# Kernel optimization log

Measured on AMD Instinct MI355X. Metric: run time of the kernel, lower is better.

The kernel has to match this reference:

```python
import jax, jax.numpy as jnp
import numpy as np

N_QUBITS = 6
N_LAYERS = 3
FEATURE_DIM = 512
ENC_HIDDEN = max(32, N_QUBITS * 4)  # 32
HEAD_HIDDEN = 128
G, T = 54, 24
DIM = 2 ** N_QUBITS  # 64


def _ry_batched(angles):
    # angles: [B] -> batched RY matrices [B, 2, 2] (complex64)
    c = jnp.cos(angles * 0.5)
    s = jnp.sin(angles * 0.5)
    U = jnp.stack([jnp.stack([c, -s], -1), jnp.stack([s, c], -1)], -2)
    return U.astype(jnp.complex64)


def _rot(phi, theta, omega):
    # PennyLane Rot = RZ(omega) RY(theta) RZ(phi); returns [2, 2] complex64
    c = jnp.cos(theta * 0.5).astype(jnp.complex64)
    s = jnp.sin(theta * 0.5).astype(jnp.complex64)
    ep = jnp.exp(-0.5j * (phi + omega).astype(jnp.complex64))  # e^{-i(phi+omega)/2}
    em = jnp.exp(-0.5j * (phi - omega).astype(jnp.complex64))  # e^{-i(phi-omega)/2}
    u00 = ep * c
    u01 = -jnp.conj(em) * s
    u10 = em * s
    u11 = jnp.conj(ep) * c
    return jnp.stack([jnp.stack([u00, u01]), jnp.stack([u10, u11])])


def _apply_1q_batched(state, U, q):
    # state: [B, 2^n]; U: [B, 2, 2] (per-sample gate, e.g. data-encoding RY)
    B = state.shape[0]
    st = state.reshape(B, 2 ** q, 2, -1)
    st = jnp.einsum('bij,bljr->blir', U, st)
    return st.reshape(B, -1)


def _apply_1q(state, U, q):
    # state: [B, 2^n]; U: [2, 2] shared across batch (trainable Rot)
    B = state.shape[0]
    st = state.reshape(B, 2 ** q, 2, -1)
    st = jnp.einsum('ij,bljr->blir', U, st)
    return st.reshape(B, -1)


def _apply_cnot(state, c, t):
    # state: [B, 2^n]; flip target axis where control bit == 1
    B = state.shape[0]
    st = state.reshape((B,) + (2,) * N_QUBITS)
    ax_c, ax_t = 1 + c, 1 + t
    s0 = jnp.take(st, 0, axis=ax_c)
    s1 = jnp.take(st, 1, axis=ax_c)
    s1 = jnp.flip(s1, axis=ax_t if ax_t < ax_c else ax_t - 1)
    st = jnp.stack([s0, s1], axis=ax_c)
    return st.reshape(B, -1)


def _expvals_z(state):
    # <Z_q> for every qubit: [B, n]
    B = state.shape[0]
    probs = (state.real ** 2 + state.imag ** 2).reshape((B,) + (2,) * N_QUBITS)
    outs = []
    for q in range(N_QUBITS):
        axes = tuple(i for i in range(1, N_QUBITS + 1) if i != q + 1)
        p = probs.sum(axes)  # [B, 2]
        outs.append(p[:, 0] - p[:, 1])
    return jnp.stack(outs, -1)


def _circuit(angles, q_weights):
    # angles: [B, n_qubits] float32; q_weights: [L, n, 3]
    B = angles.shape[0]
    state = jnp.zeros((B, DIM), jnp.complex64).at[:, 0].set(1.0)
    for layer in range(N_LAYERS):
        # data_reuploading=True -> re-encode every layer
        for q in range(N_QUBITS):
            state = _apply_1q_batched(state, _ry_batched(angles[:, q]), q)
        for q in range(N_QUBITS):
            w = q_weights[layer, q]
            state = _apply_1q(state, _rot(w[0], w[1], w[2]), q)
        for q in range(0, N_QUBITS - 1, 2):
            state = _apply_cnot(state, q, q + 1)
        for q in range(1, N_QUBITS - 1, 2):
            state = _apply_cnot(state, q, q + 1)
        state = _apply_cnot(state, N_QUBITS - 1, 0)  # n_qubits > 2
    return _expvals_z(state)


def setup_inputs() -> dict:
    key = jax.random.key(0)
    ks = jax.random.split(key, 10)
    B = 32768
    return {
        'x': jax.random.normal(ks[0], (B, FEATURE_DIM), jnp.float32),
        'enc_w1': 0.05 * jax.random.normal(ks[1], (FEATURE_DIM, ENC_HIDDEN), jnp.float32),
        'enc_b1': jnp.zeros((ENC_HIDDEN,), jnp.float32),
        'enc_w2': 0.05 * jax.random.normal(ks[2], (ENC_HIDDEN, N_QUBITS), jnp.float32),
        'enc_b2': jnp.zeros((N_QUBITS,), jnp.float32),
        'q_weights': 0.01 * jax.random.normal(ks[3], (N_LAYERS, N_QUBITS, 3), jnp.float32),
        'head_w1': 0.1 * jax.random.normal(ks[4], (N_QUBITS, HEAD_HIDDEN), jnp.float32),
        'head_b1': jnp.zeros((HEAD_HIDDEN,), jnp.float32),
        'head_w2': 0.05 * jax.random.normal(ks[5], (HEAD_HIDDEN, G * T), jnp.float32),
        'head_b2': jnp.zeros((G * T,), jnp.float32),
    }


def reference(x, enc_w1, enc_b1, enc_w2, enc_b2, q_weights,
              head_w1, head_b1, head_w2, head_b2):
    # classical encoder -> angles [B, n_qubits]
    h = jnp.tanh(x @ enc_w1 + enc_b1)
    angles = h @ enc_w2 + enc_b2
    # batched state-vector PQC simulation
    z = _circuit(angles, q_weights).astype(jnp.float32)  # [B, n_qubits]
    # classical head (dropout is identity in eval)
    g = jax.nn.relu(z @ head_w1 + head_b1)
    logits = g @ head_w2 + head_b2
    return logits.reshape(-1, G, T)
```

## Files before the change

kernel.cpp:

```cpp
#include <hip/hip_runtime.h>

typedef __bf16 bf16x8 __attribute__((ext_vector_type(8)));
typedef float floatx4 __attribute__((ext_vector_type(4)));
typedef unsigned short ushort8 __attribute__((ext_vector_type(8)));

__device__ __forceinline__ unsigned short f2bf(float f) {
    unsigned u = __float_as_uint(f);
    u += 0x7fffu + ((u >> 16) & 1u);
    return (unsigned short)(u >> 16);
}

template <int ST>
__device__ __forceinline__ void apply_local(float* fr, float* fi,
    float m00r, float m00i, float m01r, float m01i,
    float m10r, float m10i, float m11r, float m11i) {
#pragma unroll
    for (int i = 0; i < 16; ++i) {
        if ((i & ST) == 0) {
            int i1 = i + ST;
            float r0 = fr[i], u0 = fi[i], r1 = fr[i1], u1 = fi[i1];
            fr[i]  = m00r * r0 - m00i * u0 + m01r * r1 - m01i * u1;
            fi[i]  = m00r * u0 + m00i * r0 + m01r * u1 + m01i * r1;
            fr[i1] = m10r * r0 - m10i * u0 + m11r * r1 - m11i * u1;
            fi[i1] = m10r * u0 + m10i * r0 + m11r * u1 + m11i * r1;
        }
    }
}

template <int XM>
__device__ __forceinline__ void apply_cross(float* fr, float* fi, bool hi,
    float m00r, float m00i, float m01r, float m01i,
    float m10r, float m10i, float m11r, float m11i) {
    float car = hi ? m10r : m00r, cai = hi ? m10i : m00i;
    float cbr = hi ? m11r : m01r, cbi = hi ? m11i : m01i;
#pragma unroll
    for (int j = 0; j < 16; ++j) {
        float mr = fr[j], mi = fi[j];
        float pr = __shfl_xor(mr, XM);
        float pi = __shfl_xor(mi, XM);
        float a0r = hi ? pr : mr, a0i = hi ? pi : mi;
        float a1r = hi ? mr : pr, a1i = hi ? mi : pi;
        fr[j] = car * a0r - cai * a0i + cbr * a1r - cbi * a1i;
        fi[j] = car * a0i + cai * a0r + cbr * a1i + cbi * a1r;
    }
}

#define SWAP2(a, b) { float _t = fr[a]; fr[a] = fr[b]; fr[b] = _t; \
                      _t = fi[a]; fi[a] = fi[b]; fi[b] = _t; }

__global__ __launch_bounds__(256) void fused_front(
    const float* __restrict__ x, const float* __restrict__ w1,
    const float* __restrict__ b1, const float* __restrict__ w2,
    const float* __restrict__ b2, const float* __restrict__ qw,
    const float* __restrict__ hw1, const float* __restrict__ hb1,
    const float* __restrict__ hw2,
    unsigned short* __restrict__ w2t, unsigned short* __restrict__ g) {

    if (blockIdx.x >= 512) {
        int t = (blockIdx.x - 512) * 256 + threadIdx.x;
        int nn = t >> 4;
        int kc = (t & 15) * 8;
        if (nn < 1296) {
            ushort8 pk;
#pragma unroll
            for (int j = 0; j < 8; ++j) pk[j] = f2bf(hw2[(size_t)(kc + j) * 1296 + nn]);
            *(ushort8*)(w2t + (size_t)nn * 128 + kc) = pk;
        }
        return;
    }

    __shared__ float part[4][64][33];
    __shared__ float hsh[64][33];
    __shared__ float umat_s[144];
    __shared__ float casa[64][12];

    if (threadIdx.x < 18) {
        int t = threadIdx.x;
        float phi = qw[t * 3], theta = qw[t * 3 + 1], omega = qw[t * 3 + 2];
        float c = cosf(0.5f * theta), s = sinf(0.5f * theta);
        float po = 0.5f * (phi + omega), pm = 0.5f * (phi - omega);
        float epr = cosf(po), epi = -sinf(po);
        float emr = cosf(pm), emi = -sinf(pm);
        float* u = umat_s + t * 8;
        u[0] = epr * c;  u[1] = epi * c;
        u[2] = -emr * s; u[3] = emi * s;
        u[4] = emr * s;  u[5] = emi * s;
        u[6] = epr * c;  u[7] = -epi * c;
    }

    int lane = threadIdx.x & 63;
    int wave = threadIdx.x >> 6;
    int swave = __builtin_amdgcn_readfirstlane(wave);
    size_t row = (size_t)blockIdx.x * 64 + lane;
    const float2* x2 = (const float2*)(x + row * 512 + swave * 128);
    const float* wseg = w1 + swave * 128 * 32;

    float acc[32];
#pragma unroll
    for (int j = 0; j < 32; ++j) acc[j] = 0.f;

#pragma clang loop unroll(disable)
    for (int k2 = 0; k2 < 64; ++k2) {
        float2 xv = x2[k2];
        const float* wr = wseg + k2 * 64;
#pragma unroll
        for (int j = 0; j < 32; ++j) acc[j] = fmaf(wr[j], xv.x, acc[j]);
#pragma unroll
        for (int j = 0; j < 32; ++j) acc[j] = fmaf(wr[32 + j], xv.y, acc[j]);
    }
#pragma unroll
    for (int j = 0; j < 32; ++j) part[wave][lane][j] = acc[j];
    __syncthreads();

    {
        int rl = threadIdx.x & 63;
        int jg = (threadIdx.x >> 6) * 8;
#pragma unroll
        for (int jj = 0; jj < 8; ++jj) {
            int j = jg + jj;
            float v = part[0][rl][j] + part[1][rl][j] + part[2][rl][j] + part[3][rl][j] + b1[j];
            hsh[rl][j] = tanhf(v);
        }
    }
    __syncthreads();

    {
        int row_a = threadIdx.x & 63;
        for (int qq = threadIdx.x >> 6; qq < 6; qq += 4) {
            float a = b2[qq];
#pragma unroll
            for (int j = 0; j < 32; ++j) a = fmaf(hsh[row_a][j], w2[j * 6 + qq], a);
            a *= 0.5f;
            casa[row_a][qq]     = cosf(a);
            casa[row_a][qq + 6] = sinf(a);
        }
    }
    __syncthreads();

    int samp = wave * 16 + (lane & 15);
    int p = lane >> 4;
    bool podd = (p & 1) != 0;
    bool phi1 = (p >> 1) != 0;

    float ca[6], sa[6];
#pragma unroll
    for (int q = 0; q < 6; ++q) { ca[q] = casa[samp][q]; sa[q] = casa[samp][q + 6]; }

    float fr[16], fi[16];
#pragma unroll
    for (int j = 0; j < 16; ++j) { fr[j] = 0.f; fi[j] = 0.f; }
    fr[0] = (p == 0) ? 1.f : 0.f;

#pragma clang loop unroll(disable)
    for (int layer = 0; layer < 3; ++layer) {
        const float* ub = umat_s + layer * 48;
#define MAT(Q)                                                            \
        const float* u = ub + (Q) * 8;                                    \
        float c = ca[Q], ss = sa[Q];                                      \
        float m00r = u[0] * c + u[2] * ss, m00i = u[1] * c + u[3] * ss;   \
        float m01r = u[2] * c - u[0] * ss, m01i = u[3] * c - u[1] * ss;   \
        float m10r = u[4] * c + u[6] * ss, m10i = u[5] * c + u[7] * ss;   \
        float m11r = u[6] * c - u[4] * ss, m11i = u[7] * c - u[5] * ss;
        { MAT(0) apply_cross<32>(fr, fi, phi1, m00r, m00i, m01r, m01i, m10r, m10i, m11r, m11i); }
        { MAT(1) apply_cross<16>(fr, fi, podd, m00r, m00i, m01r, m01i, m10r, m10i, m11r, m11i); }
        { MAT(2) apply_local<8>(fr, fi, m00r, m00i, m01r, m01i, m10r, m10i, m11r, m11i); }
        { MAT(3) apply_local<4>(fr, fi, m00r, m00i, m01r, m01i, m10r, m10i, m11r, m11i); }
        { MAT(4) apply_local<2>(fr, fi, m00r, m00i, m01r, m01i, m10r, m10i, m11r, m11i); }
        { MAT(5) apply_local<1>(fr, fi, m00r, m00i, m01r, m01i, m10r, m10i, m11r, m11i); }
#undef MAT
#pragma unroll
        for (int j = 0; j < 16; ++j) {
            float pr = __shfl_xor(fr[j], 16);
            float pi = __shfl_xor(fi[j], 16);
            fr[j] = phi1 ? pr : fr[j];
            fi[j] = phi1 ? pi : fi[j];
        }
        SWAP2(8, 12) SWAP2(9, 13) SWAP2(10, 14) SWAP2(11, 15)
        SWAP2(2, 3) SWAP2(6, 7) SWAP2(10, 11) SWAP2(14, 15)
        {
            float tr[16], ti[16];
#pragma unroll
            for (int j = 0; j < 16; ++j) { tr[j] = fr[j]; ti[j] = fi[j]; }
#pragma unroll
            for (int j = 0; j < 16; ++j) {
                fr[j] = podd ? tr[j ^ 8] : tr[j];
                fi[j] = podd ? ti[j ^ 8] : ti[j];
            }
        }
        SWAP2(4, 6) SWAP2(5, 7) SWAP2(12, 14) SWAP2(13, 15)
#pragma unroll
        for (int j = 1; j < 16; j += 2) {
            fr[j] = __shfl_xor(fr[j], 32);
            fi[j] = __shfl_xor(fi[j], 32);
        }
    }

    float zt = 0.f, z2 = 0.f, z3 = 0.f, z4 = 0.f, z5 = 0.f;
#pragma unroll
    for (int j = 0; j < 16; ++j) {
        float pp = fr[j] * fr[j] + fi[j] * fi[j];
        zt += pp;
        z2 += (j & 8) ? -pp : pp;
        z3 += (j & 4) ? -pp : pp;
        z4 += (j & 2) ? -pp : pp;
        z5 += (j & 1) ? -pp : pp;
    }
    float zz[6];
    zz[0] = phi1 ? -zt : zt;
    zz[1] = podd ? -zt : zt;
    zz[2] = z2; zz[3] = z3; zz[4] = z4; zz[5] = z5;
#pragma unroll
    for (int q = 0; q < 6; ++q) {
        zz[q] += __shfl_xor(zz[q], 16);
        zz[q] += __shfl_xor(zz[q], 32);
    }

    int s = blockIdx.x * 64 + samp;
    unsigned short* gp = g + (size_t)s * 128 + p * 32;
#pragma unroll
    for (int j0 = 0; j0 < 32; j0 += 8) {
        ushort8 pk;
#pragma unroll
        for (int jj = 0; jj < 8; ++jj) {
            int j = p * 32 + j0 + jj;
            float a = hb1[j];
#pragma unroll
            for (int q = 0; q < 6; ++q) a = fmaf(zz[q], hw1[q * 128 + j], a);
            a = fmaxf(a, 0.f);
            pk[jj] = f2bf(a);
        }
        *(ushort8*)(gp + j0) = pk;
    }
}

__global__ __launch_bounds__(256) void head_gemm(
    const unsigned short* __restrict__ g, const unsigned short* __restrict__ w2t,
    const float* __restrict__ b2, float* __restrict__ out) {
    int lane = threadIdx.x & 63;
    int task = blockIdx.x * 4 + (threadIdx.x >> 6);
    int m = task / 27;
    int n = task - m * 27;
    int row0 = m * 64, col0 = n * 48;
    int l15 = lane & 15, quad = lane >> 4;

    const unsigned short* ap = w2t + (size_t)(col0 + l15) * 128 + quad * 8;
    const unsigned short* bp = g + (size_t)(row0 + l15) * 128 + quad * 8;

    floatx4 acc[12];
#pragma unroll
    for (int i = 0; i < 12; ++i) acc[i] = (floatx4)0.f;

#pragma unroll
    for (int ks = 0; ks < 4; ++ks) {
        bf16x8 af[3], bf[4];
#pragma unroll
        for (int t = 0; t < 3; ++t) af[t] = *(const bf16x8*)(ap + (size_t)t * 16 * 128 + ks * 32);
#pragma unroll
        for (int sub = 0; sub < 4; ++sub) bf[sub] = *(const bf16x8*)(bp + (size_t)sub * 16 * 128 + ks * 32);
#pragma unroll
        for (int t = 0; t < 3; ++t)
#pragma unroll
            for (int sub = 0; sub < 4; ++sub)
                acc[t * 4 + sub] = __builtin_amdgcn_mfma_f32_16x16x32_bf16(af[t], bf[sub], acc[t * 4 + sub], 0, 0, 0);
    }

#pragma unroll
    for (int t = 0; t < 3; ++t) {
        const float* bb = b2 + col0 + t * 16 + quad * 4;
        floatx4 bias = { bb[0], bb[1], bb[2], bb[3] };
#pragma unroll
        for (int sub = 0; sub < 4; ++sub) {
            floatx4 v = acc[t * 4 + sub] + bias;
            floatx4* dst = (floatx4*)(out + (size_t)(row0 + sub * 16 + l15) * 1296 + col0 + t * 16 + quad * 4);
            __builtin_nontemporal_store(v, dst);
        }
    }
}

extern "C" void kernel_launch(void* const* d_in, const int* in_sizes, int n_in,
                              void* d_out, int out_size, void* d_ws, size_t ws_size,
                              hipStream_t stream) {
    const float* x   = (const float*)d_in[0];
    const float* ew1 = (const float*)d_in[1];
    const float* eb1 = (const float*)d_in[2];
    const float* ew2 = (const float*)d_in[3];
    const float* eb2 = (const float*)d_in[4];
    const float* qw  = (const float*)d_in[5];
    const float* hw1 = (const float*)d_in[6];
    const float* hb1 = (const float*)d_in[7];
    const float* hw2 = (const float*)d_in[8];
    const float* hb2 = (const float*)d_in[9];
    float* out = (float*)d_out;

    char* ws = (char*)d_ws;
    unsigned short* g   = (unsigned short*)(ws);
    unsigned short* w2t = (unsigned short*)(ws + 8388608);

    fused_front<<<dim3(593), dim3(256), 0, stream>>>(x, ew1, eb1, ew2, eb2, qw, hw1, hb1, hw2, w2t, g);
    head_gemm<<<dim3(3456), dim3(256), 0, stream>>>(g, w2t, hb2, out);
}
```

Before: 342.9 us.

## Double front-kernel threads, split statevector across 8 lanes, restructure head GEMM loop

The front kernel now uses 512 threads per block. The encoder K-split goes over 8 waves, and each sample's statevector is spread over 8 lanes with 8 amplitudes each instead of 4 lanes with 16, adding one cross-lane gate and an extra permutation shuffle. The head hidden layer is recomputed after staging z in shared memory so that stores are coalesced per sample. The head GEMM now gives each block 32 rows, keeps the g fragments in registers, and loops over column tiles per wave; it also drops nontemporal stores. This trades more shuffles and a barrier for lower register pressure, higher occupancy and better reuse of g.

After: 346.8 us. About the same (+1.1%).

```diff
diff --git a/kernel.cpp b/kernel.cpp
--- a/kernel.cpp
+++ b/kernel.cpp
@@ -15,7 +15,7 @@
     float m00r, float m00i, float m01r, float m01i,
     float m10r, float m10i, float m11r, float m11i) {
 #pragma unroll
-    for (int i = 0; i < 16; ++i) {
+    for (int i = 0; i < 8; ++i) {
         if ((i & ST) == 0) {
             int i1 = i + ST;
             float r0 = fr[i], u0 = fi[i], r1 = fr[i1], u1 = fi[i1];
@@ -34,7 +34,7 @@
     float car = hi ? m10r : m00r, cai = hi ? m10i : m00i;
     float cbr = hi ? m11r : m01r, cbi = hi ? m11i : m01i;
 #pragma unroll
-    for (int j = 0; j < 16; ++j) {
+    for (int j = 0; j < 8; ++j) {
         float mr = fr[j], mi = fi[j];
         float pr = __shfl_xor(mr, XM);
         float pi = __shfl_xor(mi, XM);
@@ -48,7 +48,7 @@
 #define SWAP2(a, b) { float _t = fr[a]; fr[a] = fr[b]; fr[b] = _t; \
                       _t = fi[a]; fi[a] = fi[b]; fi[b] = _t; }
 
-__global__ __launch_bounds__(256) void fused_front(
+__global__ __launch_bounds__(512, 4) void fused_front(
     const float* __restrict__ x, const float* __restrict__ w1,
     const float* __restrict__ b1, const float* __restrict__ w2,
     const float* __restrict__ b2, const float* __restrict__ qw,
@@ -57,7 +57,7 @@
     unsigned short* __restrict__ w2t, unsigned short* __restrict__ g) {
 
     if (blockIdx.x >= 512) {
-        int t = (blockIdx.x - 512) * 256 + threadIdx.x;
+        int t = (blockIdx.x - 512) * 512 + threadIdx.x;
         int nn = t >> 4;
         int kc = (t & 15) * 8;
         if (nn < 1296) {
@@ -69,38 +69,41 @@
         return;
     }
 
-    __shared__ float part[4][64][33];
-    __shared__ float hsh[64][33];
+    __shared__ float part[8][64][33];
     __shared__ float umat_s[144];
-    __shared__ float casa[64][12];
-
-    if (threadIdx.x < 18) {
-        int t = threadIdx.x;
-        float phi = qw[t * 3], theta = qw[t * 3 + 1], omega = qw[t * 3 + 2];
+
+    float (*hsh)[33] = part[0];
+    float (*casa)[12] = (float (*)[12])part[1];
+    float (*zsh)[6]   = (float (*)[6])part[2];
+
+    int tid = threadIdx.x;
+
+    if (tid < 18) {
+        float phi = qw[tid * 3], theta = qw[tid * 3 + 1], omega = qw[tid * 3 + 2];
         float c = cosf(0.5f * theta), s = sinf(0.5f * theta);
         float po = 0.5f * (phi + omega), pm = 0.5f * (phi - omega);
         float epr = cosf(po), epi = -sinf(po);
         float emr = cosf(pm), emi = -sinf(pm);
-        float* u = umat_s + t * 8;
+        float* u = umat_s + tid * 8;
         u[0] = epr * c;  u[1] = epi * c;
         u[2] = -emr * s; u[3] = emi * s;
         u[4] = emr * s;  u[5] = emi * s;
         u[6] = epr * c;  u[7] = -epi * c;
     }
 
-    int lane = threadIdx.x & 63;
-    int wave = threadIdx.x >> 6;
+    int lane = tid & 63;
+    int wave = tid >> 6;
     int swave = __builtin_amdgcn_readfirstlane(wave);
     size_t row = (size_t)blockIdx.x * 64 + lane;
-    const float2* x2 = (const float2*)(x + row * 512 + swave * 128);
-    const float* wseg = w1 + swave * 128 * 32;
+    const float2* x2 = (const float2*)(x + row * 512 + swave * 64);
+    const float* wseg = w1 + swave * 64 * 32;
 
     float acc[32];
 #pragma unroll
     for (int j = 0; j < 32; ++j) acc[j] = 0.f;
 
 #pragma clang loop unroll(disable)
-    for (int k2 = 0; k2 < 64; ++k2) {
+    for (int k2 = 0; k2 < 32; ++k2) {
         float2 xv = x2[k2];
         const float* wr = wseg + k2 * 64;
 #pragma unroll
@@ -113,42 +116,43 @@
     __syncthreads();
 
     {
-        int rl = threadIdx.x & 63;
-        int jg = (threadIdx.x >> 6) * 8;
-#pragma unroll
-        for (int jj = 0; jj < 8; ++jj) {
+        int rl = tid & 63;
+        int jg = (tid >> 6) * 4;
+#pragma unroll
+        for (int jj = 0; jj < 4; ++jj) {
             int j = jg + jj;
-            float v = part[0][rl][j] + part[1][rl][j] + part[2][rl][j] + part[3][rl][j] + b1[j];
+            float v = b1[j];
+#pragma unroll
+            for (int w = 0; w < 8; ++w) v += part[w][rl][j];
             hsh[rl][j] = tanhf(v);
         }
     }
     __syncthreads();
 
-    {
-        int row_a = threadIdx.x & 63;
-        for (int qq = threadIdx.x >> 6; qq < 6; qq += 4) {
-            float a = b2[qq];
-#pragma unroll
-            for (int j = 0; j < 32; ++j) a = fmaf(hsh[row_a][j], w2[j * 6 + qq], a);
-            a *= 0.5f;
-            casa[row_a][qq]     = cosf(a);
-            casa[row_a][qq + 6] = sinf(a);
-        }
+    if (tid < 384) {
+        int row_a = tid & 63;
+        int q = tid >> 6;
+        float a = b2[q];
+#pragma unroll
+        for (int j = 0; j < 32; ++j) a = fmaf(hsh[row_a][j], w2[j * 6 + q], a);
+        a *= 0.5f;
+        casa[row_a][q * 2]     = cosf(a);
+        casa[row_a][q * 2 + 1] = sinf(a);
     }
     __syncthreads();
 
-    int samp = wave * 16 + (lane & 15);
-    int p = lane >> 4;
-    bool podd = (p & 1) != 0;
-    bool phi1 = (p >> 1) != 0;
+    int s8 = lane & 7;
+    int p = lane >> 3;
+    int samp = wave * 8 + s8;
+    bool pb4 = (p & 4) != 0, pb2 = (p & 2) != 0, pb1 = (p & 1) != 0;
 
     float ca[6], sa[6];
 #pragma unroll
-    for (int q = 0; q < 6; ++q) { ca[q] = casa[samp][q]; sa[q] = casa[samp][q + 6]; }
-
-    float fr[16], fi[16];
-#pragma unroll
-    for (int j = 0; j < 16; ++j) { fr[j] = 0.f; fi[j] = 0.f; }
+    for (int q = 0; q < 6; ++q) { ca[q] = casa[samp][q * 2]; sa[q] = casa[samp][q * 2 + 1]; }
+
+    float fr[8], fi[8];
+#pragma unroll
+    for (int j = 0; j < 8; ++j) { fr[j] = 0.f; fi[j] = 0.f; }
     fr[0] = (p == 0) ? 1.f : 0.f;
 
 #pragma clang loop unroll(disable)
@@ -161,71 +165,85 @@
         float m01r = u[2] * c - u[0] * ss, m01i = u[3] * c - u[1] * ss;   \
         float m10r = u[4] * c + u[6] * ss, m10i = u[5] * c + u[7] * ss;   \
         float m11r = u[6] * c - u[4] * ss, m11i = u[7] * c - u[5] * ss;
-        { MAT(0) apply_cross<32>(fr, fi, phi1, m00r, m00i, m01r, m01i, m10r, m10i, m11r, m11i); }
-        { MAT(1) apply_cross<16>(fr, fi, podd, m00r, m00i, m01r, m01i, m10r, m10i, m11r, m11i); }
-        { MAT(2) apply_local<8>(fr, fi, m00r, m00i, m01r, m01i, m10r, m10i, m11r, m11i); }
+        { MAT(0) apply_cross<32>(fr, fi, pb4, m00r, m00i, m01r, m01i, m10r, m10i, m11r, m11i); }
+        { MAT(1) apply_cross<16>(fr, fi, pb2, m00r, m00i, m01r, m01i, m10r, m10i, m11r, m11i); }
+        { MAT(2) apply_cross<8>(fr, fi, pb1, m00r, m00i, m01r, m01i, m10r, m10i, m11r, m11i); }
         { MAT(3) apply_local<4>(fr, fi, m00r, m00i, m01r, m01i, m10r, m10i, m11r, m11i); }
         { MAT(4) apply_local<2>(fr, fi, m00r, m00i, m01r, m01i, m10r, m10i, m11r, m11i); }
         { MAT(5) apply_local<1>(fr, fi, m00r, m00i, m01r, m01i, m10r, m10i, m11r, m11i); }
 #undef MAT
 #pragma unroll
-        for (int j = 0; j < 16; ++j) {
+        for (int j = 0; j < 8; ++j) {
             float pr = __shfl_xor(fr[j], 16);
             float pi = __shfl_xor(fi[j], 16);
-            fr[j] = phi1 ? pr : fr[j];
-            fi[j] = phi1 ? pi : fi[j];
-        }
-        SWAP2(8, 12) SWAP2(9, 13) SWAP2(10, 14) SWAP2(11, 15)
-        SWAP2(2, 3) SWAP2(6, 7) SWAP2(10, 11) SWAP2(14, 15)
+            fr[j] = pb4 ? pr : fr[j];
+            fi[j] = pb4 ? pi : fi[j];
+        }
         {
-            float tr[16], ti[16];
-#pragma unroll
-            for (int j = 0; j < 16; ++j) { tr[j] = fr[j]; ti[j] = fi[j]; }
-#pragma unroll
-            for (int j = 0; j < 16; ++j) {
-                fr[j] = podd ? tr[j ^ 8] : tr[j];
-                fi[j] = podd ? ti[j ^ 8] : ti[j];
+            float tr[8], ti[8];
+#pragma unroll
+            for (int j = 0; j < 8; ++j) { tr[j] = fr[j]; ti[j] = fi[j]; }
+#pragma unroll
+            for (int j = 0; j < 8; ++j) {
+                fr[j] = pb1 ? tr[j ^ 4] : tr[j];
+                fi[j] = pb1 ? ti[j ^ 4] : ti[j];
             }
         }
-        SWAP2(4, 6) SWAP2(5, 7) SWAP2(12, 14) SWAP2(13, 15)
-#pragma unroll
-        for (int j = 1; j < 16; j += 2) {
+        SWAP2(2, 3) SWAP2(6, 7)
+#pragma unroll
+        for (int j = 0; j < 8; ++j) {
+            float pr = __shfl_xor(fr[j], 8);
+            float pi = __shfl_xor(fi[j], 8);
+            fr[j] = pb2 ? pr : fr[j];
+            fi[j] = pb2 ? pi : fi[j];
+        }
+        SWAP2(4, 6) SWAP2(5, 7)
+#pragma unroll
+        for (int j = 1; j < 8; j += 2) {
             fr[j] = __shfl_xor(fr[j], 32);
             fi[j] = __shfl_xor(fi[j], 32);
         }
     }
 
-    float zt = 0.f, z2 = 0.f, z3 = 0.f, z4 = 0.f, z5 = 0.f;
-#pragma unroll
-    for (int j = 0; j < 16; ++j) {
+    float zt = 0.f, z3 = 0.f, z4 = 0.f, z5 = 0.f;
+#pragma unroll
+    for (int j = 0; j < 8; ++j) {
         float pp = fr[j] * fr[j] + fi[j] * fi[j];
         zt += pp;
-        z2 += (j & 8) ? -pp : pp;
         z3 += (j & 4) ? -pp : pp;
         z4 += (j & 2) ? -pp : pp;
         z5 += (j & 1) ? -pp : pp;
     }
     float zz[6];
-    zz[0] = phi1 ? -zt : zt;
-    zz[1] = podd ? -zt : zt;
-    zz[2] = z2; zz[3] = z3; zz[4] = z4; zz[5] = z5;
+    zz[0] = pb4 ? -zt : zt;
+    zz[1] = pb2 ? -zt : zt;
+    zz[2] = pb1 ? -zt : zt;
+    zz[3] = z3; zz[4] = z4; zz[5] = z5;
 #pragma unroll
     for (int q = 0; q < 6; ++q) {
+        zz[q] += __shfl_xor(zz[q], 8);
         zz[q] += __shfl_xor(zz[q], 16);
         zz[q] += __shfl_xor(zz[q], 32);
     }
-
-    int s = blockIdx.x * 64 + samp;
-    unsigned short* gp = g + (size_t)s * 128 + p * 32;
-#pragma unroll
-    for (int j0 = 0; j0 < 32; j0 += 8) {
+    if (p < 6) zsh[samp][p] = zz[p];
+    __syncthreads();
+
+    int samp_h = wave * 8 + (lane >> 3);
+    int seg = lane & 7;
+    float z6[6];
+#pragma unroll
+    for (int q = 0; q < 6; ++q) z6[q] = zsh[samp_h][q];
+    size_t sglob = (size_t)blockIdx.x * 64 + samp_h;
+    unsigned short* gp = g + sglob * 128 + seg * 16;
+#pragma unroll
+    for (int j0 = 0; j0 < 16; j0 += 8) {
         ushort8 pk;
 #pragma unroll
         for (int jj = 0; jj < 8; ++jj) {
-            int j = p * 32 + j0 + jj;
+            int j = seg * 16 + j0 + jj;
             float a = hb1[j];
 #pragma unroll
-            for (int q = 0; q < 6; ++q) a = fmaf(zz[q], hw1[q * 128 + j], a);
+            for (int q = 0; q < 6; ++q) a = fmaf(z6[q], hw1[q * 128 + j], a);
             a = fmaxf(a, 0.f);
             pk[jj] = f2bf(a);
         }
@@ -237,42 +255,48 @@
     const unsigned short* __restrict__ g, const unsigned short* __restrict__ w2t,
     const float* __restrict__ b2, float* __restrict__ out) {
     int lane = threadIdx.x & 63;
-    int task = blockIdx.x * 4 + (threadIdx.x >> 6);
-    int m = task / 27;
-    int n = task - m * 27;
-    int row0 = m * 64, col0 = n * 48;
+    int wv = threadIdx.x >> 6;
+    int row0 = blockIdx.x * 32;
     int l15 = lane & 15, quad = lane >> 4;
 
-    const unsigned short* ap = w2t + (size_t)(col0 + l15) * 128 + quad * 8;
     const unsigned short* bp = g + (size_t)(row0 + l15) * 128 + quad * 8;
-
-    floatx4 acc[12];
-#pragma unroll
-    for (int i = 0; i < 12; ++i) acc[i] = (floatx4)0.f;
-
-#pragma unroll
-    for (int ks = 0; ks < 4; ++ks) {
-        bf16x8 af[3], bf[4];
-#pragma unroll
-        for (int t = 0; t < 3; ++t) af[t] = *(const bf16x8*)(ap + (size_t)t * 16 * 128 + ks * 32);
-#pragma unroll
-        for (int sub = 0; sub < 4; ++sub) bf[sub] = *(const bf16x8*)(bp + (size_t)sub * 16 * 128 + ks * 32);
-#pragma unroll
-        for (int t = 0; t < 3; ++t)
-#pragma unroll
-            for (int sub = 0; sub < 4; ++sub)
-                acc[t * 4 + sub] = __builtin_amdgcn_mfma_f32_16x16x32_bf16(af[t], bf[sub], acc[t * 4 + sub], 0, 0, 0);
-    }
-
-#pragma unroll
-    for (int t = 0; t < 3; ++t) {
-        const float* bb = b2 + col0 + t * 16 + quad * 4;
-        floatx4 bias = { bb[0], bb[1], bb[2], bb[3] };
-#pragma unroll
-        for (int sub = 0; sub < 4; ++sub) {
-            floatx4 v = acc[t * 4 + sub] + bias;
-            floatx4* dst = (floatx4*)(out + (size_t)(row0 + sub * 16 + l15) * 1296 + col0 + t * 16 + quad * 4);
-            __builtin_nontemporal_store(v, dst);
+    bf16x8 bfr[2][4];
+#pragma unroll
+    for (int sub = 0; sub < 2; ++sub)
+#pragma unroll
+        for (int ks = 0; ks < 4; ++ks)
+            bfr[sub][ks] = *(const bf16x8*)(bp + (size_t)sub * 16 * 128 + ks * 32);
+
+    for (int n = wv; n < 27; n += 4) {
+        int col0 = n * 48;
+        const unsigned short* ap = w2t + (size_t)(col0 + l15) * 128 + quad * 8;
+
+        floatx4 acc[6];
+#pragma unroll
+        for (int i = 0; i < 6; ++i) acc[i] = (floatx4)0.f;
+
+#pragma unroll
+        for (int ks = 0; ks < 4; ++ks) {
+            bf16x8 af[3];
+#pragma unroll
+            for (int t = 0; t < 3; ++t) af[t] = *(const bf16x8*)(ap + (size_t)t * 16 * 128 + ks * 32);
+#pragma unroll
+            for (int t = 0; t < 3; ++t)
+#pragma unroll
+                for (int sub = 0; sub < 2; ++sub)
+                    acc[t * 2 + sub] = __builtin_amdgcn_mfma_f32_16x16x32_bf16(af[t], bfr[sub][ks], acc[t * 2 + sub], 0, 0, 0);
+        }
+
+#pragma unroll
+        for (int t = 0; t < 3; ++t) {
+            const float* bb = b2 + col0 + t * 16 + quad * 4;
+            floatx4 bias = { bb[0], bb[1], bb[2], bb[3] };
+#pragma unroll
+            for (int sub = 0; sub < 2; ++sub) {
+                floatx4 v = acc[t * 2 + sub] + bias;
+                floatx4* dst = (floatx4*)(out + (size_t)(row0 + sub * 16 + l15) * 1296 + col0 + t * 16 + quad * 4);
+                *dst = v;
+            }
         }
     }
 }
@@ -296,6 +320,6 @@
     unsigned short* g   = (unsigned short*)(ws);
     unsigned short* w2t = (unsigned short*)(ws + 8388608);
 
-    fused_front<<<dim3(593), dim3(256), 0, stream>>>(x, ew1, eb1, ew2, eb2, qw, hw1, hb1, hw2, w2t, g);
-    head_gemm<<<dim3(3456), dim3(256), 0, stream>>>(g, w2t, hb2, out);
-}
+    fused_front<<<dim3(553), dim3(512), 0, stream>>>(x, ew1, eb1, ew2, eb2, qw, hw1, hb1, hw2, w2t, g);
+    head_gemm<<<dim3(1024), dim3(256), 0, stream>>>(g, w2t, hb2, out);
+}
```
